# Optimization experiments

Hardware: AMD Instinct MI355X
Metric: run time of the kernel (lower is better)

## Reference

```python
import jax, jax.numpy as jnp
import numpy as np

B, S, D, H = 2, 4096, 256, 8
P = 64               # proj_dim_l
R = S // P           # proj_dim_r = 64, P*R == S
DH = D // H          # head_dim = 32


def setup_inputs() -> dict:
    key = jax.random.key(0)
    kx, kl, kr, kv, ko = jax.random.split(key, 5)
    scale = 0.05  # stand-in for xavier-uniform scale
    x  = jax.random.normal(kx, (B, S, D), dtype=jnp.float32)
    Wl = jax.random.normal(kl, (D, P), dtype=jnp.float32) * scale
    Wr = jax.random.normal(kr, (D, R), dtype=jnp.float32) * scale
    Wv = jax.random.normal(kv, (D, D), dtype=jnp.float32) * scale
    Wo = jax.random.normal(ko, (D, D), dtype=jnp.float32) * scale
    return {"x": x, "Wl": Wl, "Wr": Wr, "Wv": Wv, "Wo": Wo}


def reference(x, Wl, Wr, Wv, Wo):
    b, s, d = x.shape
    # value projection + head split -> (b, H, S, DH). Dropout p=0 (eval) = identity.
    v = (x @ Wv).reshape(b, s, H, DH).transpose(0, 2, 1, 3)
    # factorized score: row n is vec(outer(l_n, r_n)) of length P*R == S
    l = x @ Wl                                   # (b, S, P)
    r = x @ Wr                                   # (b, S, R)
    attn = (l[:, :, :, None] * r[:, :, None, :]).reshape(b, s, s)  # (b, S, S)
    score = jax.nn.softmax(attn, axis=-1)        # (b, S, S)
    # shared score across heads, per-head value matmul
    o = jnp.einsum('bnm,bhmd->bhnd', score, v)   # (b, H, S, DH)
    o = o.transpose(0, 2, 1, 3).reshape(b, s, d) # concat heads
    return o @ Wo
```

## Files before the change

kernel.cpp:

```cpp
#include <hip/hip_runtime.h>
#include <hip/hip_bf16.h>

typedef __attribute__((ext_vector_type(8))) __bf16 bf16x8;
typedef __attribute__((ext_vector_type(4))) __bf16 bf16x4;
typedef __attribute__((ext_vector_type(4))) float  f32x4;

#define MFMA16(a, b, c) __builtin_amdgcn_mfma_f32_16x16x32_bf16((a), (b), (c), 0, 0, 0)

static constexpr size_t OFF_WOT  = 0;
static constexpr size_t OFF_VT   = 1u << 20;
static constexpr size_t OFF_L    = 6u << 20;
static constexpr size_t OFF_R    = 8u << 20;
static constexpr size_t OFF_PART = 10u << 20;
static constexpr size_t OFF_ZP   = 26u << 20;

__device__ __forceinline__ float fast_exp2(float x) {
  float e;
  asm("v_exp_f32 %0, %1" : "=v"(e) : "v"(x));
  return e;
}

__device__ __forceinline__ bf16x8 cvt8(float4 a, float4 b) {
  bf16x8 o;
  o[0] = (__bf16)a.x; o[1] = (__bf16)a.y; o[2] = (__bf16)a.z; o[3] = (__bf16)a.w;
  o[4] = (__bf16)b.x; o[5] = (__bf16)b.y; o[6] = (__bf16)b.z; o[7] = (__bf16)b.w;
  return o;
}

__global__ __launch_bounds__(256) void k_proj(const float* __restrict__ x,
                                              const float* __restrict__ Wv,
                                              const float* __restrict__ Wl,
                                              const float* __restrict__ Wr,
                                              const float* __restrict__ Wo,
                                              __bf16* __restrict__ Vt,
                                              float* __restrict__ lbuf,
                                              float* __restrict__ rbuf,
                                              __bf16* __restrict__ Wot) {
  __shared__ __align__(16) __bf16 wt[64 * 264];
  __shared__ __align__(16) __bf16 vs[8 * 64 * 8];
  const int t = threadIdx.x;
  const int lane = t & 63, wave = t >> 6;
  const int l16 = lane & 15, quad = lane >> 4;
  const int wr = wave >> 1, wc = wave & 1;
  const int rbk = blockIdx.x;
  const int ct  = blockIdx.y;
  const float* Wsrc;
  int wstride, colbase;
  if (ct < 4)       { Wsrc = Wv; wstride = 256; colbase = ct * 64; }
  else if (ct == 4) { Wsrc = Wl; wstride = 64;  colbase = 0; }
  else              { Wsrc = Wr; wstride = 64;  colbase = 0; }

  if (ct >= 4) {
    const int j = ((ct - 4) * 128 + rbk) * 256 + t;
    const int k = j >> 8, n = j & 255;
    Wot[n * 256 + k] = (__bf16)Wo[j];
  }

  {
    const int kr = t >> 4;
    const int n4 = (t & 15) * 4;
#pragma unroll
    for (int kk = 0; kk < 16; ++kk) {
      const int k = kk * 16 + kr;
      float4 v = *(const float4*)(Wsrc + (size_t)k * wstride + colbase + n4);
      wt[(n4 + 0) * 264 + k] = (__bf16)v.x;
      wt[(n4 + 1) * 264 + k] = (__bf16)v.y;
      wt[(n4 + 2) * 264 + k] = (__bf16)v.z;
      wt[(n4 + 3) * 264 + k] = (__bf16)v.w;
    }
  }
  __syncthreads();

  const int row0 = rbk * 64 + wr * 32;
  const int c0l  = wc * 32;
  f32x4 acc[2][2] = {};
  for (int kk = 0; kk < 256; kk += 32) {
    const int ko = kk + quad * 8;
    const float* xr0 = x + (size_t)(row0 + l16) * 256 + ko;
    const float* xr1 = x + (size_t)(row0 + 16 + l16) * 256 + ko;
    bf16x8 a0 = cvt8(*(const float4*)xr0, *(const float4*)(xr0 + 4));
    bf16x8 a1 = cvt8(*(const float4*)xr1, *(const float4*)(xr1 + 4));
    bf16x8 b0 = *(const bf16x8*)(wt + (c0l + l16) * 264 + ko);
    bf16x8 b1 = *(const bf16x8*)(wt + (c0l + 16 + l16) * 264 + ko);
    acc[0][0] = MFMA16(a0, b0, acc[0][0]);
    acc[0][1] = MFMA16(a0, b1, acc[0][1]);
    acc[1][0] = MFMA16(a1, b0, acc[1][0]);
    acc[1][1] = MFMA16(a1, b1, acc[1][1]);
  }
  if (ct < 4) {
#pragma unroll
    for (int mt = 0; mt < 2; ++mt)
#pragma unroll
      for (int nt = 0; nt < 2; ++nt) {
        const int m8 = wr * 4 + mt * 2 + (quad >> 1);
        const int d  = wc * 32 + nt * 16 + l16;
        bf16x4 o;
        o.x = (__bf16)acc[mt][nt][0];
        o.y = (__bf16)acc[mt][nt][1];
        o.z = (__bf16)acc[mt][nt][2];
        o.w = (__bf16)acc[mt][nt][3];
        *(bf16x4*)(&vs[m8 * 512 + d * 8 + (quad & 1) * 4]) = o;
      }
    __syncthreads();
    const int m8 = t >> 5, s32 = t & 31;
    const int bat = rbk >> 6, mc = rbk & 63;
    bf16x8 a = *(const bf16x8*)(&vs[m8 * 512 + s32 * 16]);
    bf16x8 b = *(const bf16x8*)(&vs[m8 * 512 + s32 * 16 + 8]);
    __bf16* dst = Vt + (size_t)bat * 1048576 + (size_t)mc * 16384 +
                  m8 * 2048 + ct * 512 + s32 * 16;
    *(bf16x8*)dst       = a;
    *(bf16x8*)(dst + 8) = b;
  } else {
    float* dstb = (ct == 4) ? lbuf : rbuf;
#pragma unroll
    for (int mt = 0; mt < 2; ++mt)
#pragma unroll
      for (int nt = 0; nt < 2; ++nt) {
        const int col = c0l + nt * 16 + l16;
        const int gr  = rbk * 64 + wr * 32 + mt * 16 + quad * 4;
#pragma unroll
        for (int rr = 0; rr < 4; ++rr)
          dstb[(size_t)(gr + rr) * 64 + col] = acc[mt][nt][rr];
      }
  }
}

__global__ __launch_bounds__(512, 2) void k_attn(const float* __restrict__ lbuf,
                                                 const float* __restrict__ rbuf,
                                                 const __bf16* __restrict__ Vt,
                                                 __bf16* __restrict__ part,
                                                 float* __restrict__ zpart) {
  __shared__ __align__(16) char smem[74240];
  __bf16* vt0 = (__bf16*)smem;
  __bf16* vt1 = (__bf16*)(smem + 32768);
  float*  ls  = (float*)(smem + 65536);
  const int t = threadIdx.x;
  const int lane = t & 63, w = t >> 6;
  const int l16 = lane & 15, quad = lane >> 4;
  const int wr = w >> 2, wc = w & 3;
  const int rb = blockIdx.x;
  const int sp = blockIdx.y;
  const int g0 = rb * 128;
  const int bat = rb >> 5;
  const __bf16* Vbase = Vt + (size_t)bat * 1048576;
  const int ck0 = sp * 16;

  {
    const int idx = t * 4;
    const int row = idx >> 4, c = idx & 15;
    f32x4 v = *(const f32x4*)(lbuf + (size_t)(g0 + row) * 64 + ck0 + c);
    ls[row * 17 + c + 0] = v[0];
    ls[row * 17 + c + 1] = v[1];
    ls[row * 17 + c + 2] = v[2];
    ls[row * 17 + c + 3] = v[3];
  }
  const float LOG2E = 1.44269504088896f;
  float rreg[4][16];
#pragma unroll
  for (int mt = 0; mt < 4; ++mt) {
    const float* rp = rbuf + (size_t)(g0 + wr * 64 + mt * 16 + l16) * 64;
    f32x4 a = *(const f32x4*)(rp + quad * 8);
    f32x4 b = *(const f32x4*)(rp + quad * 8 + 4);
    f32x4 c = *(const f32x4*)(rp + 32 + quad * 8);
    f32x4 d = *(const f32x4*)(rp + 32 + quad * 8 + 4);
#pragma unroll
    for (int j = 0; j < 4; ++j) {
      rreg[mt][j]      = a[j] * LOG2E;
      rreg[mt][4 + j]  = b[j] * LOG2E;
      rreg[mt][8 + j]  = c[j] * LOG2E;
      rreg[mt][12 + j] = d[j] * LOG2E;
    }
  }

  f32x4 acc[4][4] = {};
  float zacc[4] = {0.f, 0.f, 0.f, 0.f};
  bf16x8 stg[4];

  {
    const __bf16* src = Vbase + (size_t)ck0 * 16384;
#pragma unroll
    for (int i = 0; i < 4; ++i) stg[i] = *(const bf16x8*)(src + (size_t)(i * 512 + t) * 8);
#pragma unroll
    for (int i = 0; i < 4; ++i) *(bf16x8*)(vt0 + (i * 512 + t) * 8) = stg[i];
  }
  __syncthreads();

  for (int kc = 0; kc < 16; ++kc) {
    __bf16* cur = (kc & 1) ? vt1 : vt0;
    __bf16* nxt = (kc & 1) ? vt0 : vt1;
    if (kc < 15) {
      const __bf16* src = Vbase + (size_t)(ck0 + kc + 1) * 16384;
#pragma unroll
      for (int i = 0; i < 4; ++i) stg[i] = *(const bf16x8*)(src + (size_t)(i * 512 + t) * 8);
    }
    bf16x8 af[4][2];
#pragma unroll
    for (int mt = 0; mt < 4; ++mt) {
      const float lv = ls[(wr * 64 + mt * 16 + l16) * 17 + kc];
#pragma unroll
      for (int kk = 0; kk < 2; ++kk)
#pragma unroll
        for (int j = 0; j < 8; ++j) {
          const float e = fast_exp2(lv * rreg[mt][kk * 8 + j]);
          zacc[mt] += e;
          af[mt][kk][j] = (__bf16)e;
        }
    }
#pragma unroll
    for (int kk = 0; kk < 2; ++kk)
#pragma unroll
      for (int nt = 0; nt < 4; ++nt) {
        bf16x8 bv = *(const bf16x8*)(cur + (kk * 4 + quad) * 2048 +
                                     (wc * 64 + nt * 16 + l16) * 8);
        acc[0][nt] = MFMA16(af[0][kk], bv, acc[0][nt]);
        acc[1][nt] = MFMA16(af[1][kk], bv, acc[1][nt]);
        acc[2][nt] = MFMA16(af[2][kk], bv, acc[2][nt]);
        acc[3][nt] = MFMA16(af[3][kk], bv, acc[3][nt]);
      }
    if (kc < 15) {
#pragma unroll
      for (int i = 0; i < 4; ++i) *(bf16x8*)(nxt + (i * 512 + t) * 8) = stg[i];
    }
    __syncthreads();
  }

#pragma unroll
  for (int mt = 0; mt < 4; ++mt) {
    float z = zacc[mt];
    z += __shfl_xor(z, 16);
    z += __shfl_xor(z, 32);
    if (wc == 0 && quad == 0)
      zpart[(size_t)sp * 8192 + g0 + wr * 64 + mt * 16 + l16] = z;
  }

  __bf16* ctile = (__bf16*)smem;
#pragma unroll
  for (int mt = 0; mt < 4; ++mt)
#pragma unroll
    for (int nt = 0; nt < 4; ++nt) {
      const int r0 = wr * 64 + mt * 16 + quad * 4;
      const int c  = wc * 64 + nt * 16 + l16;
#pragma unroll
      for (int rr = 0; rr < 4; ++rr)
        ctile[(r0 + rr) * 264 + c] = (__bf16)acc[mt][nt][rr];
    }
  __syncthreads();
  __bf16* pb = part + (size_t)sp * (8192 * 256);
#pragma unroll
  for (int p = 0; p < 8; ++p) {
    const int u = p * 512 + t;
    const int row = u >> 5, seg = u & 31;
    *(bf16x8*)(pb + (size_t)(g0 + row) * 256 + seg * 8) =
        *(const bf16x8*)(ctile + row * 264 + seg * 8);
  }
}

__global__ __launch_bounds__(256) void k_outfix(const __bf16* __restrict__ part,
                                                const float* __restrict__ zpart,
                                                const __bf16* __restrict__ Wot,
                                                float* __restrict__ out) {
  const int t = threadIdx.x;
  const int lane = t & 63, w = t >> 6;
  const int l16 = lane & 15, quad = lane >> 4;
  const int wr = w >> 1, wc = w & 1;
  const int rb = blockIdx.x;
  const int arow = rb * 32 + wr * 16 + l16;
  float z = 0.f;
#pragma unroll
  for (int s = 0; s < 4; ++s) z += zpart[(size_t)s * 8192 + arow];
  const float iz = 1.0f / z;
  f32x4 acc[8] = {};
#pragma unroll 2
  for (int ks = 0; ks < 8; ++ks) {
    const int k0 = ks * 32 + quad * 8;
    float sum[8] = {};
#pragma unroll
    for (int s = 0; s < 4; ++s) {
      bf16x8 p = *(const bf16x8*)(part + (size_t)s * (8192 * 256) + (size_t)arow * 256 + k0);
#pragma unroll
      for (int j = 0; j < 8; ++j) sum[j] += (float)p[j];
    }
    bf16x8 afr;
#pragma unroll
    for (int j = 0; j < 8; ++j) afr[j] = (__bf16)(sum[j] * iz);
#pragma unroll
    for (int nt = 0; nt < 8; ++nt) {
      bf16x8 bv = *(const bf16x8*)(Wot + (size_t)(wc * 128 + nt * 16 + l16) * 256 + k0);
      acc[nt] = MFMA16(afr, bv, acc[nt]);
    }
  }
#pragma unroll
  for (int nt = 0; nt < 8; ++nt) {
    const int col = wc * 128 + nt * 16 + l16;
    const int r0  = rb * 32 + wr * 16 + quad * 4;
#pragma unroll
    for (int rr = 0; rr < 4; ++rr)
      out[(size_t)(r0 + rr) * 256 + col] = acc[nt][rr];
  }
}

extern "C" void kernel_launch(void* const* d_in, const int* in_sizes, int n_in,
                              void* d_out, int out_size, void* d_ws, size_t ws_size,
                              hipStream_t stream) {
  const float* x  = (const float*)d_in[0];
  const float* Wl = (const float*)d_in[1];
  const float* Wr = (const float*)d_in[2];
  const float* Wv = (const float*)d_in[3];
  const float* Wo = (const float*)d_in[4];
  char* ws = (char*)d_ws;
  __bf16* Wot = (__bf16*)(ws + OFF_WOT);
  __bf16* Vt  = (__bf16*)(ws + OFF_VT);
  float*  lb  = (float*)(ws + OFF_L);
  float*  rbf = (float*)(ws + OFF_R);
  __bf16* prt = (__bf16*)(ws + OFF_PART);
  float*  zp  = (float*)(ws + OFF_ZP);
  float*  out = (float*)d_out;

  k_proj<<<dim3(128, 6), 256, 0, stream>>>(x, Wv, Wl, Wr, Wo, Vt, lb, rbf, Wot);
  k_attn<<<dim3(64, 4), 512, 0, stream>>>(lb, rbf, Vt, prt, zp);
  k_outfix<<<256, 256, 0, stream>>>(prt, zp, Wot, out);
}
```

Before: 137.1 us.

## Split attention value columns across two blocks to double grid size

The attention kernel now splits the 256 value columns into two halves across a new grid dimension. It uses 256-thread blocks, so the grid grows from 256 to 512 blocks for better CU occupancy. Each block processes two key chunks per loop iteration with a halved V tile. The trade-off is that the exp/softmax score computation is duplicated in both column halves, doubling the transcendental work per output.

```diff
diff --git a/kernel.cpp b/kernel.cpp
--- a/kernel.cpp
+++ b/kernel.cpp
@@ -125,7 +125,7 @@
   }
 }
 
-__global__ __launch_bounds__(512, 2) void k_attn(const float* __restrict__ lbuf,
+__global__ __launch_bounds__(256, 2) void k_attn(const float* __restrict__ lbuf,
                                                  const float* __restrict__ rbuf,
                                                  const __bf16* __restrict__ Vt,
                                                  __bf16* __restrict__ part,
@@ -137,22 +137,24 @@
   const int t = threadIdx.x;
   const int lane = t & 63, w = t >> 6;
   const int l16 = lane & 15, quad = lane >> 4;
-  const int wr = w >> 2, wc = w & 3;
+  const int wr = w >> 1, wc = w & 1;
   const int rb = blockIdx.x;
-  const int sp = blockIdx.y;
+  const int cb = blockIdx.y;
+  const int sp = blockIdx.z;
   const int g0 = rb * 128;
   const int bat = rb >> 5;
-  const __bf16* Vbase = Vt + (size_t)bat * 1048576;
-  const int ck0 = sp * 16;
+  const __bf16* Vbase = Vt + (size_t)bat * 1048576 + cb * 1024;
+  const int mc0 = sp * 16;
 
   {
-    const int idx = t * 4;
-    const int row = idx >> 4, c = idx & 15;
-    f32x4 v = *(const f32x4*)(lbuf + (size_t)(g0 + row) * 64 + ck0 + c);
-    ls[row * 17 + c + 0] = v[0];
-    ls[row * 17 + c + 1] = v[1];
-    ls[row * 17 + c + 2] = v[2];
-    ls[row * 17 + c + 3] = v[3];
+    const int row = t >> 1, c8 = (t & 1) * 8;
+    f32x4 a = *(const f32x4*)(lbuf + (size_t)(g0 + row) * 64 + mc0 + c8);
+    f32x4 b = *(const f32x4*)(lbuf + (size_t)(g0 + row) * 64 + mc0 + c8 + 4);
+#pragma unroll
+    for (int i = 0; i < 4; ++i) {
+      ls[row * 17 + c8 + i]     = a[i];
+      ls[row * 17 + c8 + 4 + i] = b[i];
+    }
   }
   const float LOG2E = 1.44269504088896f;
   float rreg[4][16];
@@ -174,62 +176,71 @@
 
   f32x4 acc[4][4] = {};
   float zacc[4] = {0.f, 0.f, 0.f, 0.f};
-  bf16x8 stg[4];
+  bf16x8 stg[8];
+
+#define SRCP(MC, U) (Vbase + (size_t)((MC) + ((U) >> 10)) * 16384 + \
+                     (((U) >> 7) & 7) * 2048 + ((U) & 127) * 8)
 
   {
-    const __bf16* src = Vbase + (size_t)ck0 * 16384;
-#pragma unroll
-    for (int i = 0; i < 4; ++i) stg[i] = *(const bf16x8*)(src + (size_t)(i * 512 + t) * 8);
-#pragma unroll
-    for (int i = 0; i < 4; ++i) *(bf16x8*)(vt0 + (i * 512 + t) * 8) = stg[i];
+#pragma unroll
+    for (int i = 0; i < 8; ++i) stg[i] = *(const bf16x8*)SRCP(mc0, i * 256 + t);
+#pragma unroll
+    for (int i = 0; i < 8; ++i) *(bf16x8*)(vt0 + (i * 256 + t) * 8) = stg[i];
   }
   __syncthreads();
 
-  for (int kc = 0; kc < 16; ++kc) {
+  for (int kc = 0; kc < 8; ++kc) {
     __bf16* cur = (kc & 1) ? vt1 : vt0;
     __bf16* nxt = (kc & 1) ? vt0 : vt1;
-    if (kc < 15) {
-      const __bf16* src = Vbase + (size_t)(ck0 + kc + 1) * 16384;
-#pragma unroll
-      for (int i = 0; i < 4; ++i) stg[i] = *(const bf16x8*)(src + (size_t)(i * 512 + t) * 8);
-    }
-    bf16x8 af[4][2];
+    if (kc < 7) {
+      const int mcn = mc0 + (kc + 1) * 2;
+#pragma unroll
+      for (int i = 0; i < 8; ++i) stg[i] = *(const bf16x8*)SRCP(mcn, i * 256 + t);
+    }
+    float lv2[4][2];
 #pragma unroll
     for (int mt = 0; mt < 4; ++mt) {
-      const float lv = ls[(wr * 64 + mt * 16 + l16) * 17 + kc];
-#pragma unroll
-      for (int kk = 0; kk < 2; ++kk)
+      const int rbase = (wr * 64 + mt * 16 + l16) * 17 + kc * 2;
+      lv2[mt][0] = ls[rbase];
+      lv2[mt][1] = ls[rbase + 1];
+    }
+#pragma unroll
+    for (int kp = 0; kp < 4; ++kp) {
+      bf16x8 af[4];
+#pragma unroll
+      for (int mt = 0; mt < 4; ++mt) {
+        const float lv = lv2[mt][kp >> 1];
 #pragma unroll
         for (int j = 0; j < 8; ++j) {
-          const float e = fast_exp2(lv * rreg[mt][kk * 8 + j]);
+          const float e = fast_exp2(lv * rreg[mt][(kp & 1) * 8 + j]);
           zacc[mt] += e;
-          af[mt][kk][j] = (__bf16)e;
+          af[mt][j] = (__bf16)e;
         }
-    }
-#pragma unroll
-    for (int kk = 0; kk < 2; ++kk)
+      }
 #pragma unroll
       for (int nt = 0; nt < 4; ++nt) {
-        bf16x8 bv = *(const bf16x8*)(cur + (kk * 4 + quad) * 2048 +
-                                     (wc * 64 + nt * 16 + l16) * 8);
-        acc[0][nt] = MFMA16(af[0][kk], bv, acc[0][nt]);
-        acc[1][nt] = MFMA16(af[1][kk], bv, acc[1][nt]);
-        acc[2][nt] = MFMA16(af[2][kk], bv, acc[2][nt]);
-        acc[3][nt] = MFMA16(af[3][kk], bv, acc[3][nt]);
+        bf16x8 bv = *(const bf16x8*)(cur + ((kp * 4 + quad) * 128 +
+                                            wc * 64 + nt * 16 + l16) * 8);
+        acc[0][nt] = MFMA16(af[0], bv, acc[0][nt]);
+        acc[1][nt] = MFMA16(af[1], bv, acc[1][nt]);
+        acc[2][nt] = MFMA16(af[2], bv, acc[2][nt]);
+        acc[3][nt] = MFMA16(af[3], bv, acc[3][nt]);
       }
-    if (kc < 15) {
-#pragma unroll
-      for (int i = 0; i < 4; ++i) *(bf16x8*)(nxt + (i * 512 + t) * 8) = stg[i];
+    }
+    if (kc < 7) {
+#pragma unroll
+      for (int i = 0; i < 8; ++i) *(bf16x8*)(nxt + (i * 256 + t) * 8) = stg[i];
     }
     __syncthreads();
   }
+#undef SRCP
 
 #pragma unroll
   for (int mt = 0; mt < 4; ++mt) {
     float z = zacc[mt];
     z += __shfl_xor(z, 16);
     z += __shfl_xor(z, 32);
-    if (wc == 0 && quad == 0)
+    if (cb == 0 && wc == 0 && quad == 0)
       zpart[(size_t)sp * 8192 + g0 + wr * 64 + mt * 16 + l16] = z;
   }
 
@@ -242,16 +253,16 @@
       const int c  = wc * 64 + nt * 16 + l16;
 #pragma unroll
       for (int rr = 0; rr < 4; ++rr)
-        ctile[(r0 + rr) * 264 + c] = (__bf16)acc[mt][nt][rr];
+        ctile[(r0 + rr) * 136 + c] = (__bf16)acc[mt][nt][rr];
     }
   __syncthreads();
-  __bf16* pb = part + (size_t)sp * (8192 * 256);
+  __bf16* pb = part + (size_t)sp * (8192 * 256) + cb * 128;
 #pragma unroll
   for (int p = 0; p < 8; ++p) {
-    const int u = p * 512 + t;
-    const int row = u >> 5, seg = u & 31;
+    const int u = p * 256 + t;
+    const int row = u >> 4, seg = u & 15;
     *(bf16x8*)(pb + (size_t)(g0 + row) * 256 + seg * 8) =
-        *(const bf16x8*)(ctile + row * 264 + seg * 8);
+        *(const bf16x8*)(ctile + row * 136 + seg * 8);
   }
 }
 
@@ -317,6 +328,6 @@
   float*  out = (float*)d_out;
 
   k_proj<<<dim3(128, 6), 256, 0, stream>>>(x, Wv, Wl, Wr, Wo, Vt, lb, rbf, Wot);
-  k_attn<<<dim3(64, 4), 512, 0, stream>>>(lb, rbf, Vt, prt, zp);
+  k_attn<<<dim3(64, 2, 4), 256, 0, stream>>>(lb, rbf, Vt, prt, zp);
   k_outfix<<<256, 256, 0, stream>>>(prt, zp, Wot, out);
 }
```

New measurement: 214.9 us. 1.57x slower.
